# Performance work log

Measured on AMD Instinct MI355X. Metric: run time of the kernel, lower is better.

The kernel has to match this reference:

```python
import jax, jax.numpy as jnp
import numpy as np

S, B, H = 2048, 64, 1024


def setup_inputs() -> dict:
    key = jax.random.key(0)
    k1, k2, k3 = jax.random.split(key, 3)
    scale = 1.0 / np.sqrt(H)
    return {
        "hidden": jax.random.normal(k1, (1, B, H), dtype=jnp.float32),
        "encoder_outputs": jax.random.normal(k2, (S, B, H), dtype=jnp.float32),
        "W_attn": jax.random.normal(k3, (H, H), dtype=jnp.float32) * scale,
        "b_attn": jnp.zeros((H,), dtype=jnp.float32),
    }


def reference(hidden, encoder_outputs, W_attn, b_attn):
    # method == 'general':
    #   energy[s,b,:] = W_attn @ enc[s,b,:] + b_attn   (nn.Linear: x @ W^T + b)
    #   score[b,s]   = hidden[0,b,:] . energy[s,b,:]
    energy = jnp.einsum("sbh,kh->sbk", encoder_outputs, W_attn) + b_attn  # [S,B,H]
    scores = jnp.einsum("bh,sbh->bs", hidden[0], energy)                  # [B,S]
    return jax.nn.softmax(scores, axis=1)[:, None, :]                     # [B,1,S]
```

## Files before the change

### kernel.cpp

```cpp
#include <hip/hip_runtime.h>
#include <hip/hip_bf16.h>
#include <math.h>

#define S_DIM 2048
#define B_DIM 64
#define H_DIM 1024
#define KP     16
#define KCHUNK (H_DIM / KP)
#define BLK_B  4

typedef float f32x4 __attribute__((ext_vector_type(4)));

__global__ __launch_bounds__(256) void v_partial_kernel(
    const float* __restrict__ hidden,
    const float* __restrict__ W,
    float* __restrict__ partial)
{
    const int p   = blockIdx.x;
    const int b0  = blockIdx.y * BLK_B;
    const int tid = threadIdx.x;
    const int h0  = tid * 4;
    const int k0  = p * KCHUNK;

    __shared__ float s_hid[BLK_B][KCHUNK];
    {
        const int bb = tid / KCHUNK;
        const int kk = tid % KCHUNK;
        s_hid[bb][kk] = hidden[(size_t)(b0 + bb) * H_DIM + k0 + kk];
    }
    __syncthreads();

    f32x4 acc[BLK_B];
#pragma unroll
    for (int bb = 0; bb < BLK_B; ++bb) acc[bb] = (f32x4)0.f;

#pragma unroll 4
    for (int k = 0; k < KCHUNK; ++k) {
        const f32x4 w = *reinterpret_cast<const f32x4*>(W + (size_t)(k0 + k) * H_DIM + h0);
#pragma unroll
        for (int bb = 0; bb < BLK_B; ++bb) {
            const float hk = s_hid[bb][k];
            acc[bb].x = fmaf(hk, w.x, acc[bb].x);
            acc[bb].y = fmaf(hk, w.y, acc[bb].y);
            acc[bb].z = fmaf(hk, w.z, acc[bb].z);
            acc[bb].w = fmaf(hk, w.w, acc[bb].w);
        }
    }

#pragma unroll
    for (int bb = 0; bb < BLK_B; ++bb)
        *reinterpret_cast<f32x4*>(partial + ((size_t)p * B_DIM + b0 + bb) * H_DIM + h0) = acc[bb];
}

__global__ __launch_bounds__(256) void v_reduce_kernel(
    const float* __restrict__ partial,
    float* __restrict__ v)
{
    const int b   = blockIdx.x;
    const int tid = threadIdx.x;
    const int h0  = tid * 4;

    f32x4 s = (f32x4)0.f;
#pragma unroll
    for (int p = 0; p < KP; ++p)
        s += *reinterpret_cast<const f32x4*>(partial + ((size_t)p * B_DIM + b) * H_DIM + h0);
    *reinterpret_cast<f32x4*>(v + (size_t)b * H_DIM + h0) = s;
}

__global__ __launch_bounds__(256) void scores_kernel(
    const float* __restrict__ enc,
    const float* __restrict__ v,
    float* __restrict__ scores)
{
    const int b      = blockIdx.y;
    const int wave   = threadIdx.x >> 6;
    const int lane   = threadIdx.x & 63;
    const int s_base = blockIdx.x * 64 + wave * 16;

    const float* vb = v + (size_t)b * H_DIM;
    const int o = lane * 4;
    const f32x4 v0 = *reinterpret_cast<const f32x4*>(vb + o);
    const f32x4 v1 = *reinterpret_cast<const f32x4*>(vb + o + 256);
    const f32x4 v2 = *reinterpret_cast<const f32x4*>(vb + o + 512);
    const f32x4 v3 = *reinterpret_cast<const f32x4*>(vb + o + 768);

    const size_t srow = (size_t)B_DIM * H_DIM;

    for (int i = 0; i < 16; i += 4) {
        const float* ra = enc + ((size_t)(s_base + i) * B_DIM + b) * H_DIM;
        const float* rb = ra + srow;
        const float* rc = rb + srow;
        const float* rd = rc + srow;

        const f32x4 a0 = __builtin_nontemporal_load(reinterpret_cast<const f32x4*>(ra + o));
        const f32x4 a1 = __builtin_nontemporal_load(reinterpret_cast<const f32x4*>(ra + o + 256));
        const f32x4 a2 = __builtin_nontemporal_load(reinterpret_cast<const f32x4*>(ra + o + 512));
        const f32x4 a3 = __builtin_nontemporal_load(reinterpret_cast<const f32x4*>(ra + o + 768));
        const f32x4 b0 = __builtin_nontemporal_load(reinterpret_cast<const f32x4*>(rb + o));
        const f32x4 b1 = __builtin_nontemporal_load(reinterpret_cast<const f32x4*>(rb + o + 256));
        const f32x4 b2 = __builtin_nontemporal_load(reinterpret_cast<const f32x4*>(rb + o + 512));
        const f32x4 b3 = __builtin_nontemporal_load(reinterpret_cast<const f32x4*>(rb + o + 768));
        const f32x4 c0 = __builtin_nontemporal_load(reinterpret_cast<const f32x4*>(rc + o));
        const f32x4 c1 = __builtin_nontemporal_load(reinterpret_cast<const f32x4*>(rc + o + 256));
        const f32x4 c2 = __builtin_nontemporal_load(reinterpret_cast<const f32x4*>(rc + o + 512));
        const f32x4 c3 = __builtin_nontemporal_load(reinterpret_cast<const f32x4*>(rc + o + 768));
        const f32x4 d0 = __builtin_nontemporal_load(reinterpret_cast<const f32x4*>(rd + o));
        const f32x4 d1 = __builtin_nontemporal_load(reinterpret_cast<const f32x4*>(rd + o + 256));
        const f32x4 d2 = __builtin_nontemporal_load(reinterpret_cast<const f32x4*>(rd + o + 512));
        const f32x4 d3 = __builtin_nontemporal_load(reinterpret_cast<const f32x4*>(rd + o + 768));

        float acc_a = v0.x * a0.x + v0.y * a0.y + v0.z * a0.z + v0.w * a0.w
                    + v1.x * a1.x + v1.y * a1.y + v1.z * a1.z + v1.w * a1.w
                    + v2.x * a2.x + v2.y * a2.y + v2.z * a2.z + v2.w * a2.w
                    + v3.x * a3.x + v3.y * a3.y + v3.z * a3.z + v3.w * a3.w;
        float acc_b = v0.x * b0.x + v0.y * b0.y + v0.z * b0.z + v0.w * b0.w
                    + v1.x * b1.x + v1.y * b1.y + v1.z * b1.z + v1.w * b1.w
                    + v2.x * b2.x + v2.y * b2.y + v2.z * b2.z + v2.w * b2.w
                    + v3.x * b3.x + v3.y * b3.y + v3.z * b3.z + v3.w * b3.w;
        float acc_c = v0.x * c0.x + v0.y * c0.y + v0.z * c0.z + v0.w * c0.w
                    + v1.x * c1.x + v1.y * c1.y + v1.z * c1.z + v1.w * c1.w
                    + v2.x * c2.x + v2.y * c2.y + v2.z * c2.z + v2.w * c2.w
                    + v3.x * c3.x + v3.y * c3.y + v3.z * c3.z + v3.w * c3.w;
        float acc_d = v0.x * d0.x + v0.y * d0.y + v0.z * d0.z + v0.w * d0.w
                    + v1.x * d1.x + v1.y * d1.y + v1.z * d1.z + v1.w * d1.w
                    + v2.x * d2.x + v2.y * d2.y + v2.z * d2.z + v2.w * d2.w
                    + v3.x * d3.x + v3.y * d3.y + v3.z * d3.z + v3.w * d3.w;

#pragma unroll
        for (int off = 32; off > 0; off >>= 1) {
            acc_a += __shfl_xor(acc_a, off);
            acc_b += __shfl_xor(acc_b, off);
            acc_c += __shfl_xor(acc_c, off);
            acc_d += __shfl_xor(acc_d, off);
        }

        if (lane == 0) {
            float* sp = scores + (size_t)b * S_DIM + s_base + i;
            sp[0] = acc_a;
            sp[1] = acc_b;
            sp[2] = acc_c;
            sp[3] = acc_d;
        }
    }
}

__global__ __launch_bounds__(256) void softmax_kernel(
    const float* __restrict__ scores,
    float* __restrict__ out)
{
    const int b   = blockIdx.x;
    const int tid = threadIdx.x;
    const float* row = scores + (size_t)b * S_DIM;

    f32x4 va = *reinterpret_cast<const f32x4*>(row + tid * 8);
    f32x4 vb = *reinterpret_cast<const f32x4*>(row + tid * 8 + 4);

    float m = fmaxf(fmaxf(fmaxf(va.x, va.y), fmaxf(va.z, va.w)),
                    fmaxf(fmaxf(vb.x, vb.y), fmaxf(vb.z, vb.w)));

    __shared__ float red[256];
    red[tid] = m;
    __syncthreads();
    for (int off = 128; off > 0; off >>= 1) {
        if (tid < off) red[tid] = fmaxf(red[tid], red[tid + off]);
        __syncthreads();
    }
    m = red[0];
    __syncthreads();

    va.x = __expf(va.x - m); va.y = __expf(va.y - m);
    va.z = __expf(va.z - m); va.w = __expf(va.w - m);
    vb.x = __expf(vb.x - m); vb.y = __expf(vb.y - m);
    vb.z = __expf(vb.z - m); vb.w = __expf(vb.w - m);
    const float sum = va.x + va.y + va.z + va.w + vb.x + vb.y + vb.z + vb.w;

    red[tid] = sum;
    __syncthreads();
    for (int off = 128; off > 0; off >>= 1) {
        if (tid < off) red[tid] += red[tid + off];
        __syncthreads();
    }
    const float inv = 1.0f / red[0];
    __syncthreads();

    va *= inv;
    vb *= inv;
    *reinterpret_cast<f32x4*>(out + (size_t)b * S_DIM + tid * 8)     = va;
    *reinterpret_cast<f32x4*>(out + (size_t)b * S_DIM + tid * 8 + 4) = vb;
}

extern "C" void kernel_launch(void* const* d_in, const int* in_sizes, int n_in,
                              void* d_out, int out_size, void* d_ws, size_t ws_size,
                              hipStream_t stream) {
    const float* hidden = (const float*)d_in[0];
    const float* enc    = (const float*)d_in[1];
    const float* W      = (const float*)d_in[2];
    float* out          = (float*)d_out;

    float* ws      = (float*)d_ws;
    float* partial = ws;
    float* v       = partial + (size_t)KP * B_DIM * H_DIM;
    float* scores  = v + (size_t)B_DIM * H_DIM;

    v_partial_kernel<<<dim3(KP, B_DIM / BLK_B), dim3(256), 0, stream>>>(hidden, W, partial);
    v_reduce_kernel<<<dim3(B_DIM), dim3(256), 0, stream>>>(partial, v);
    scores_kernel<<<dim3(S_DIM / 64, B_DIM), dim3(256), 0, stream>>>(enc, v, scores);
    softmax_kernel<<<dim3(B_DIM), dim3(256), 0, stream>>>(scores, out);
}
```

Before: 101.0 us.

## Fuse v partial and reduce kernels into single in-block split-K kernel

Replaces the two-kernel computation of v = W^T·hidden, which wrote a 16-way partial buffer to global memory and reduced it in a second launch, with one kernel. That kernel splits K across 8 waves inside a block and reduces the partial sums through shared memory. This removes a kernel launch and the global round trip of the partial buffer. In exchange each block stages all of hidden for its 4 batches in LDS and reads W with scalar per-lane loads. The scores kernel also now writes its four results as one vector store.

```diff
diff --git a/kernel.cpp b/kernel.cpp
--- a/kernel.cpp
+++ b/kernel.cpp
@@ -5,66 +5,64 @@
 #define S_DIM 2048
 #define B_DIM 64
 #define H_DIM 1024
-#define KP     16
-#define KCHUNK (H_DIM / KP)
+#define HC     64
 #define BLK_B  4
 
 typedef float f32x4 __attribute__((ext_vector_type(4)));
 
-__global__ __launch_bounds__(256) void v_partial_kernel(
+__global__ __launch_bounds__(512) void v_kernel(
     const float* __restrict__ hidden,
     const float* __restrict__ W,
-    float* __restrict__ partial)
-{
-    const int p   = blockIdx.x;
-    const int b0  = blockIdx.y * BLK_B;
-    const int tid = threadIdx.x;
-    const int h0  = tid * 4;
-    const int k0  = p * KCHUNK;
-
-    __shared__ float s_hid[BLK_B][KCHUNK];
-    {
-        const int bb = tid / KCHUNK;
-        const int kk = tid % KCHUNK;
-        s_hid[bb][kk] = hidden[(size_t)(b0 + bb) * H_DIM + k0 + kk];
-    }
-    __syncthreads();
-
-    f32x4 acc[BLK_B];
-#pragma unroll
-    for (int bb = 0; bb < BLK_B; ++bb) acc[bb] = (f32x4)0.f;
-
-#pragma unroll 4
-    for (int k = 0; k < KCHUNK; ++k) {
-        const f32x4 w = *reinterpret_cast<const f32x4*>(W + (size_t)(k0 + k) * H_DIM + h0);
-#pragma unroll
-        for (int bb = 0; bb < BLK_B; ++bb) {
-            const float hk = s_hid[bb][k];
-            acc[bb].x = fmaf(hk, w.x, acc[bb].x);
-            acc[bb].y = fmaf(hk, w.y, acc[bb].y);
-            acc[bb].z = fmaf(hk, w.z, acc[bb].z);
-            acc[bb].w = fmaf(hk, w.w, acc[bb].w);
-        }
-    }
-
-#pragma unroll
-    for (int bb = 0; bb < BLK_B; ++bb)
-        *reinterpret_cast<f32x4*>(partial + ((size_t)p * B_DIM + b0 + bb) * H_DIM + h0) = acc[bb];
-}
-
-__global__ __launch_bounds__(256) void v_reduce_kernel(
-    const float* __restrict__ partial,
     float* __restrict__ v)
 {
-    const int b   = blockIdx.x;
-    const int tid = threadIdx.x;
-    const int h0  = tid * 4;
-
-    f32x4 s = (f32x4)0.f;
+    const int h0   = blockIdx.x * HC;
+    const int b0   = blockIdx.y * BLK_B;
+    const int tid  = threadIdx.x;
+    const int wave = tid >> 6;
+    const int lane = tid & 63;
+    const int h    = h0 + lane;
+
+    __shared__ float s_hidT[H_DIM][BLK_B];
+    {
+        const int i  = tid * 8;
+        const int bb = i >> 10;
+        const int kk = i & (H_DIM - 1);
+        const f32x4 lo = *reinterpret_cast<const f32x4*>(hidden + (size_t)(b0 + bb) * H_DIM + kk);
+        const f32x4 hi = *reinterpret_cast<const f32x4*>(hidden + (size_t)(b0 + bb) * H_DIM + kk + 4);
+        s_hidT[kk + 0][bb] = lo.x; s_hidT[kk + 1][bb] = lo.y;
+        s_hidT[kk + 2][bb] = lo.z; s_hidT[kk + 3][bb] = lo.w;
+        s_hidT[kk + 4][bb] = hi.x; s_hidT[kk + 5][bb] = hi.y;
+        s_hidT[kk + 6][bb] = hi.z; s_hidT[kk + 7][bb] = hi.w;
+    }
+    __syncthreads();
+
+    const int k0 = wave * (H_DIM / 8);
+    f32x4 acc = (f32x4)0.f;
+#pragma unroll 8
+    for (int k = 0; k < H_DIM / 8; ++k) {
+        const float w  = W[(size_t)(k0 + k) * H_DIM + h];
+        const f32x4 hv = *reinterpret_cast<const f32x4*>(&s_hidT[k0 + k][0]);
+        acc.x = fmaf(hv.x, w, acc.x);
+        acc.y = fmaf(hv.y, w, acc.y);
+        acc.z = fmaf(hv.z, w, acc.z);
+        acc.w = fmaf(hv.w, w, acc.w);
+    }
+
+    __shared__ float red[8][BLK_B][HC];
+    red[wave][0][lane] = acc.x;
+    red[wave][1][lane] = acc.y;
+    red[wave][2][lane] = acc.z;
+    red[wave][3][lane] = acc.w;
+    __syncthreads();
+
+    if (tid < BLK_B * HC) {
+        const int bb = tid >> 6;
+        const int l  = tid & 63;
+        float s = 0.f;
 #pragma unroll
-    for (int p = 0; p < KP; ++p)
-        s += *reinterpret_cast<const f32x4*>(partial + ((size_t)p * B_DIM + b) * H_DIM + h0);
-    *reinterpret_cast<f32x4*>(v + (size_t)b * H_DIM + h0) = s;
+        for (int w2 = 0; w2 < 8; ++w2) s += red[w2][bb][l];
+        v[(size_t)(b0 + bb) * H_DIM + h0 + l] = s;
+    }
 }
 
 __global__ __launch_bounds__(256) void scores_kernel(
@@ -135,11 +133,8 @@
         }
 
         if (lane == 0) {
-            float* sp = scores + (size_t)b * S_DIM + s_base + i;
-            sp[0] = acc_a;
-            sp[1] = acc_b;
-            sp[2] = acc_c;
-            sp[3] = acc_d;
+            f32x4 r; r.x = acc_a; r.y = acc_b; r.z = acc_c; r.w = acc_d;
+            *reinterpret_cast<f32x4*>(scores + (size_t)b * S_DIM + s_base + i) = r;
         }
     }
 }
@@ -197,13 +192,11 @@
     const float* W      = (const float*)d_in[2];
     float* out          = (float*)d_out;
 
-    float* ws      = (float*)d_ws;
-    float* partial = ws;
-    float* v       = partial + (size_t)KP * B_DIM * H_DIM;
-    float* scores  = v + (size_t)B_DIM * H_DIM;
-
-    v_partial_kernel<<<dim3(KP, B_DIM / BLK_B), dim3(256), 0, stream>>>(hidden, W, partial);
-    v_reduce_kernel<<<dim3(B_DIM), dim3(256), 0, stream>>>(partial, v);
+    float* ws     = (float*)d_ws;
+    float* v      = ws;
+    float* scores = v + (size_t)B_DIM * H_DIM;
+
+    v_kernel<<<dim3(H_DIM / HC, B_DIM / BLK_B), dim3(512), 0, stream>>>(hidden, W, v);
     scores_kernel<<<dim3(S_DIM / 64, B_DIM), dim3(256), 0, stream>>>(enc, v, scores);
     softmax_kernel<<<dim3(B_DIM), dim3(256), 0, stream>>>(scores, out);
 }
```

Result: faster. 97.94 us (median of 2 runs) (-3.0%).
